# Performance work log

Measured on AMD Instinct MI355X. Metric: run time of the kernel, lower is better.

The kernel has to match this reference:

```python
import jax, jax.numpy as jnp
import numpy as np

N_NODES = 30000
IN_DIM = 8
HIDDEN = 64
HEADS1 = 8
OUT_DIM = 8
NEG_SLOPE = 0.2


def _glorot(key, shape):
    fan_in, fan_out = shape[0], shape[-1]
    lim = jnp.sqrt(6.0 / (fan_in + fan_out))
    return jax.random.uniform(key, shape, jnp.float32, -lim, lim)


def setup_inputs() -> dict:
    key = jax.random.key(0)
    ks = jax.random.split(key, 12)
    x = jax.random.normal(ks[0], (N_NODES, IN_DIM), jnp.float32)
    edge_index = jax.random.randint(ks[1], (2, 300000), 0, N_NODES, jnp.int32)
    # layer 1: in=8, out=HIDDEN per head, 8 heads, concat
    W1l = _glorot(ks[2], (IN_DIM, HEADS1 * HIDDEN))
    W1r = _glorot(ks[3], (IN_DIM, HEADS1 * HIDDEN))
    a1 = _glorot(ks[4], (HEADS1, HIDDEN))
    b1 = jnp.zeros((HEADS1 * HIDDEN,), jnp.float32)
    # layer 2: in=HEADS1*HIDDEN, out=OUT_DIM, 1 head
    W2l = _glorot(ks[5], (HEADS1 * HIDDEN, OUT_DIM))
    W2r = _glorot(ks[6], (HEADS1 * HIDDEN, OUT_DIM))
    a2 = _glorot(ks[7], (1, OUT_DIM))
    b2 = jnp.zeros((OUT_DIM,), jnp.float32)
    return {"x": x, "edge_index": edge_index, "W1l": W1l, "W1r": W1r,
            "a1": a1, "b1": b1, "W2l": W2l, "W2r": W2r, "a2": a2, "b2": b2}


def gatv2_layer(x, src, dst, Wl, Wr, att, bias, heads, out_ch):
    n = x.shape[0]
    xl = (x @ Wl).reshape(n, heads, out_ch)   # messages (source side)
    xr = (x @ Wr).reshape(n, heads, out_ch)   # target side
    h = jax.nn.leaky_relu(xl[src] + xr[dst], NEG_SLOPE)   # [E,H,C]
    e = jnp.einsum('ehc,hc->eh', h, att)                  # [E,H]
    # segment softmax over incoming edges per destination node
    m = jax.ops.segment_max(e, dst, num_segments=n)
    p = jnp.exp(e - m[dst])
    denom = jax.ops.segment_sum(p, dst, num_segments=n)
    alpha = p / denom[dst]                                # [E,H]
    out = jax.ops.segment_sum(alpha[..., None] * xl[src], dst, num_segments=n)
    return out.reshape(n, heads * out_ch) + bias


def reference(x, edge_index, W1l, W1r, a1, b1, W2l, W2r, a2, b2):
    n = x.shape[0]
    loops = jnp.arange(n, dtype=edge_index.dtype)
    src = jnp.concatenate([edge_index[0], loops])  # add_self_loops=True (PyG default)
    dst = jnp.concatenate([edge_index[1], loops])
    h = gatv2_layer(x, src, dst, W1l, W1r, a1, b1, HEADS1, HIDDEN)
    h = jax.nn.relu(h)
    out = gatv2_layer(h, src, dst, W2l, W2r, a2, b2, 1, OUT_DIM)
    return out
```

## Files before the change

kernel.cpp:

```cpp
#include <hip/hip_runtime.h>
#include <hip/hip_fp16.h>
#include <math.h>

#define N_NODES   30000
#define N_EDGE    300000
#define N_EDGE_T  330000
#define HEADS     8
#define HIDDEN    64
#define IN_DIM    8
#define OUT_DIM   8
#define NEG_SLOPE 0.2f

#define DPP_ADDF(x, ctrl)                                                     \
    x += __int_as_float(__builtin_amdgcn_update_dpp(                          \
            0, __float_as_int(x), (ctrl), 0xF, 0xF, true))
#define RED16(x) do { DPP_ADDF(x, 0xB1); DPP_ADDF(x, 0x4E);                   \
                      DPP_ADDF(x, 0x141); DPP_ADDF(x, 0x140); } while (0)
#define RED8(x)  do { DPP_ADDF(x, 0xB1); DPP_ADDF(x, 0x4E);                   \
                      DPP_ADDF(x, 0x141); } while (0)


__global__ __launch_bounds__(256) void zero_kernel(int* __restrict__ count) {
    int i = blockIdx.x * 256 + threadIdx.x;
    if (i < N_NODES) count[i] = 0;
}

__global__ __launch_bounds__(256) void count_kernel(const int* __restrict__ ei,
                                                    int* __restrict__ count) {
    int e = blockIdx.x * 256 + threadIdx.x;
    if (e >= N_EDGE_T) return;
    int d = (e < N_EDGE) ? ei[N_EDGE + e] : (e - N_EDGE);
    atomicAdd(&count[d], 1);
}

__global__ __launch_bounds__(1024) void scan_kernel(const int* __restrict__ count,
                                                    int* __restrict__ row_start,
                                                    int* __restrict__ cursor) {
    __shared__ int wsum[16];
    const int tid  = threadIdx.x;
    const int wave = tid >> 6;
    const int lane = tid & 63;
    const int4* c4 = (const int4*)count;
    const int N4 = N_NODES / 4;
    int run = 0;
    for (int r = 0; r < 4; ++r) {
        const int g  = r * 1024 + tid;
        const int i0 = 2 * g;
        const int i1 = 2 * g + 1;
        int4 v0 = make_int4(0,0,0,0), v1 = make_int4(0,0,0,0);
        if (i0 < N4) v0 = c4[i0];
        if (i1 < N4) v1 = c4[i1];
        int s = v0.x + v0.y + v0.z + v0.w + v1.x + v1.y + v1.z + v1.w;
        int sc = s;
        #pragma unroll
        for (int off = 1; off < 64; off <<= 1) {
            int t = __shfl_up(sc, off, 64);
            if (lane >= off) sc += t;
        }
        if (lane == 63) wsum[wave] = sc;
        __syncthreads();
        if (tid < 16) {
            int w = wsum[tid];
            #pragma unroll
            for (int off = 1; off < 16; off <<= 1) {
                int t = __shfl_up(w, off, 64);
                if (tid >= off) w += t;
            }
            wsum[tid] = w;
        }
        __syncthreads();
        const int woff = (wave > 0) ? wsum[wave - 1] : 0;
        int e0 = run + woff + (sc - s);
        int4 ex0, ex1;
        ex0.x = e0;           ex0.y = ex0.x + v0.x;
        ex0.z = ex0.y + v0.y; ex0.w = ex0.z + v0.z;
        int e4 = ex0.w + v0.w;
        ex1.x = e4;           ex1.y = ex1.x + v1.x;
        ex1.z = ex1.y + v1.y; ex1.w = ex1.z + v1.z;
        if (i0 < N4) { ((int4*)row_start)[i0] = ex0; ((int4*)cursor)[i0] = ex0; }
        if (i1 < N4) { ((int4*)row_start)[i1] = ex1; ((int4*)cursor)[i1] = ex1; }
        const int tot = wsum[15];
        __syncthreads();
        run += tot;
    }
    if (tid == 0) row_start[N_NODES] = run;
}

__global__ __launch_bounds__(256) void scatter_kernel(const int* __restrict__ ei,
                                                      int* __restrict__ cursor,
                                                      int* __restrict__ edge_src) {
    int e = blockIdx.x * 256 + threadIdx.x;
    if (e >= N_EDGE_T) return;
    int s, d;
    if (e < N_EDGE) { s = ei[e]; d = ei[N_EDGE + e]; }
    else            { s = d = e - N_EDGE; }
    int pos = atomicAdd(&cursor[d], 1);
    edge_src[pos] = s;
}


__global__ __launch_bounds__(256) void proj_kernel(
    const float* __restrict__ x, const float* __restrict__ W1l,
    __half* __restrict__ xl_h)
{
    const int t = threadIdx.x;
    float w0[IN_DIM], w1[IN_DIM];
    #pragma unroll
    for (int k = 0; k < IN_DIM; ++k) {
        const float2 wp = *(const float2*)&W1l[k * 512 + 2 * t];
        w0[k] = wp.x; w1[k] = wp.y;
    }
    for (int n = blockIdx.x; n < N_NODES; n += gridDim.x) {
        float xv[IN_DIM];
        #pragma unroll
        for (int k = 0; k < IN_DIM; ++k) xv[k] = x[n * IN_DIM + k];
        float l0 = 0.f, l1 = 0.f;
        #pragma unroll
        for (int k = 0; k < IN_DIM; ++k) {
            l0 = fmaf(xv[k], w0[k], l0);
            l1 = fmaf(xv[k], w1[k], l1);
        }
        ((__half2*)xl_h)[n * 256 + t] = __floats2half2_rn(l0, l1);
    }
}


__global__ void __launch_bounds__(256, 4)
layer1_kernel(
    const float* __restrict__ x,
    const __half* __restrict__ xl_h, const float* __restrict__ W1r,
    const float* __restrict__ a1,  const float* __restrict__ b1,
    const float* __restrict__ W2l, const float* __restrict__ W2r,
    const int* __restrict__ row_start, const int* __restrict__ edge_src,
    float* __restrict__ xl2, float* __restrict__ xr2)
{
    const int wv   = threadIdx.x >> 6;
    const int lane = threadIdx.x & 63;
    const int d    = blockIdx.x * 4 + wv;
    const int colb = lane * 8;

    float av[8], xr[8];
    { const float4 a0 = *(const float4*)&a1[colb];
      const float4 a4 = *(const float4*)&a1[colb + 4];
      av[0]=a0.x; av[1]=a0.y; av[2]=a0.z; av[3]=a0.w;
      av[4]=a4.x; av[5]=a4.y; av[6]=a4.z; av[7]=a4.w; }
    #pragma unroll
    for (int i = 0; i < 8; ++i) xr[i] = 0.f;
    #pragma unroll
    for (int k = 0; k < IN_DIM; ++k) {
        const float4 r0 = *(const float4*)&W1r[k * 512 + colb];
        const float4 r4 = *(const float4*)&W1r[k * 512 + colb + 4];
        const float xv = x[d * IN_DIM + k];
        xr[0] = fmaf(xv, r0.x, xr[0]); xr[1] = fmaf(xv, r0.y, xr[1]);
        xr[2] = fmaf(xv, r0.z, xr[2]); xr[3] = fmaf(xv, r0.w, xr[3]);
        xr[4] = fmaf(xv, r4.x, xr[4]); xr[5] = fmaf(xv, r4.y, xr[5]);
        xr[6] = fmaf(xv, r4.z, xr[6]); xr[7] = fmaf(xv, r4.w, xr[7]);
    }

    const int rs = row_start[d];
    const int re = row_start[d + 1];

    float denom  = 0.f;
    float acc[8] = {0.f,0.f,0.f,0.f,0.f,0.f,0.f,0.f};

    auto ldrow = [&](int s, float (&o)[8]) {
        const int4 r = *(const int4*)(xl_h + (size_t)s * 512 + colb);
        union { int i; __half2 h; } u0, u1, u2, u3;
        u0.i = r.x; u1.i = r.y; u2.i = r.z; u3.i = r.w;
        float2 f;
        f = __half22float2(u0.h); o[0] = f.x; o[1] = f.y;
        f = __half22float2(u1.h); o[2] = f.x; o[3] = f.y;
        f = __half22float2(u2.h); o[4] = f.x; o[5] = f.y;
        f = __half22float2(u3.h); o[6] = f.x; o[7] = f.y;
    };

    auto edge1 = [&](const float (&rr)[8], bool valid) {
        float e = 0.f;
        #pragma unroll
        for (int i = 0; i < 8; ++i) {
            const float q = rr[i] + xr[i];
            const float t = fmaxf(q, NEG_SLOPE * q);
            e = fmaf(av[i], t, e);
        }
        RED8(e);
        const float p = valid ? __expf(e) : 0.f;
        denom += p;
        #pragma unroll
        for (int i = 0; i < 8; ++i) acc[i] = fmaf(p, rr[i], acc[i]);
    };

    float RA[8], RB[8];
    {
        const int sA = edge_src[rs];
        const bool vB0 = rs + 1 < re;
        const int sB = edge_src[vB0 ? rs + 1 : rs];
        ldrow(sA, RA); ldrow(sB, RB);
    }
    bool vB = rs + 1 < re;

    for (int base = rs;;) {
        const int  nb   = base + 2;
        const bool more = nb < re;
        float RC[8], RD[8];
        bool vD = false;
        if (more) {
            const int sC = edge_src[nb];
            vD = nb + 1 < re;
            const int sD = edge_src[vD ? nb + 1 : nb];
            ldrow(sC, RC); ldrow(sD, RD);
        }
        edge1(RA, true);
        edge1(RB, vB);
        if (!more) break;
        #pragma unroll
        for (int i = 0; i < 8; ++i) { RA[i] = RC[i]; RB[i] = RD[i]; }
        vB = vD;
        base = nb;
    }

    const float inv = 1.f / denom;
    float hv[8];
    { const float4 b0 = *(const float4*)&b1[colb];
      const float4 b4 = *(const float4*)&b1[colb + 4];
      hv[0] = fmaxf(fmaf(acc[0], inv, b0.x), 0.f);
      hv[1] = fmaxf(fmaf(acc[1], inv, b0.y), 0.f);
      hv[2] = fmaxf(fmaf(acc[2], inv, b0.z), 0.f);
      hv[3] = fmaxf(fmaf(acc[3], inv, b0.w), 0.f);
      hv[4] = fmaxf(fmaf(acc[4], inv, b4.x), 0.f);
      hv[5] = fmaxf(fmaf(acc[5], inv, b4.y), 0.f);
      hv[6] = fmaxf(fmaf(acc[6], inv, b4.z), 0.f);
      hv[7] = fmaxf(fmaf(acc[7], inv, b4.w), 0.f); }

    float vl[OUT_DIM], vr[OUT_DIM];
    #pragma unroll
    for (int j = 0; j < OUT_DIM; ++j) { vl[j] = 0.f; vr[j] = 0.f; }
    #pragma unroll
    for (int i = 0; i < 8; ++i) {
        const int c = colb + i;
        const float4 l0 = *(const float4*)&W2l[c * OUT_DIM];
        const float4 l1 = *(const float4*)&W2l[c * OUT_DIM + 4];
        const float4 r0 = *(const float4*)&W2r[c * OUT_DIM];
        const float4 r1 = *(const float4*)&W2r[c * OUT_DIM + 4];
        const float h = hv[i];
        vl[0] = fmaf(h, l0.x, vl[0]); vl[1] = fmaf(h, l0.y, vl[1]);
        vl[2] = fmaf(h, l0.z, vl[2]); vl[3] = fmaf(h, l0.w, vl[3]);
        vl[4] = fmaf(h, l1.x, vl[4]); vl[5] = fmaf(h, l1.y, vl[5]);
        vl[6] = fmaf(h, l1.z, vl[6]); vl[7] = fmaf(h, l1.w, vl[7]);
        vr[0] = fmaf(h, r0.x, vr[0]); vr[1] = fmaf(h, r0.y, vr[1]);
        vr[2] = fmaf(h, r0.z, vr[2]); vr[3] = fmaf(h, r0.w, vr[3]);
        vr[4] = fmaf(h, r1.x, vr[4]); vr[5] = fmaf(h, r1.y, vr[5]);
        vr[6] = fmaf(h, r1.z, vr[6]); vr[7] = fmaf(h, r1.w, vr[7]);
    }
    #pragma unroll
    for (int j = 0; j < OUT_DIM; ++j) {
        RED16(vl[j]);
        vl[j] += __shfl_xor(vl[j], 16, 64);
        vl[j] += __shfl_xor(vl[j], 32, 64);
        RED16(vr[j]);
        vr[j] += __shfl_xor(vr[j], 16, 64);
        vr[j] += __shfl_xor(vr[j], 32, 64);
    }
    if (lane == 0) {
        *(float4*)&xl2[d * OUT_DIM]     = make_float4(vl[0], vl[1], vl[2], vl[3]);
        *(float4*)&xl2[d * OUT_DIM + 4] = make_float4(vl[4], vl[5], vl[6], vl[7]);
        *(float4*)&xr2[d * OUT_DIM]     = make_float4(vr[0], vr[1], vr[2], vr[3]);
        *(float4*)&xr2[d * OUT_DIM + 4] = make_float4(vr[4], vr[5], vr[6], vr[7]);
    }
}


__global__ __launch_bounds__(256) void layer2_kernel(
    const float* __restrict__ xl2, const float* __restrict__ xr2,
    const float* __restrict__ a2,  const float* __restrict__ b2,
    const int* __restrict__ row_start, const int* __restrict__ edge_src,
    float* __restrict__ out)
{
    const int wave = threadIdx.x >> 6;
    const int lane = threadIdx.x & 63;
    const int d = blockIdx.x * 4 + wave;
    if (d >= N_NODES) return;
    const int sub = lane >> 3;
    const int c   = lane & 7;

    const float a_c  = a2[c];
    const float xr_d = xr2[d * OUT_DIM + c];

    const int rs = row_start[d];
    const int re = row_start[d + 1];

    int  e0 = rs + sub;      const bool v0 = e0 < re; e0 = v0 ? e0 : re - 1;
    int  e1 = rs + 8 + sub;  const bool v1 = e1 < re; e1 = v1 ? e1 : re - 1;
    const int s0 = edge_src[e0];
    const int s1 = edge_src[e1];
    const float x0 = xl2[s0 * OUT_DIM + c];
    const float x1 = xl2[s1 * OUT_DIM + c];

    const float u0 = x0 + xr_d; const float t0 = fmaxf(u0, NEG_SLOPE * u0);
    const float u1 = x1 + xr_d; const float t1 = fmaxf(u1, NEG_SLOPE * u1);
    float g0 = a_c * t0;
    float g1 = a_c * t1;
    RED8(g0); RED8(g1);
    const float p0 = v0 ? __expf(g0) : 0.f;
    const float p1 = v1 ? __expf(g1) : 0.f;
    float denom = p0 + p1;
    float acc   = fmaf(p1, x1, p0 * x0);

    for (int b = rs + 16; b < re; b += 8) {
        int e = b + sub;
        const bool v = e < re; e = v ? e : re - 1;
        const int s = edge_src[e];
        const float xs = xl2[s * OUT_DIM + c];
        const float u = xs + xr_d;
        const float t = fmaxf(u, NEG_SLOPE * u);
        float g = a_c * t;
        RED8(g);
        const float p = v ? __expf(g) : 0.f;
        denom += p;
        acc = fmaf(p, xs, acc);
    }

    denom += __shfl_xor(denom, 8,  64);  acc += __shfl_xor(acc, 8,  64);
    denom += __shfl_xor(denom, 16, 64);  acc += __shfl_xor(acc, 16, 64);
    denom += __shfl_xor(denom, 32, 64);  acc += __shfl_xor(acc, 32, 64);

    if (sub == 0) out[d * OUT_DIM + c] = acc / denom + b2[c];
}


extern "C" void kernel_launch(void* const* d_in, const int* in_sizes, int n_in,
                              void* d_out, int out_size, void* d_ws, size_t ws_size,
                              hipStream_t stream) {
    const float* x   = (const float*)d_in[0];
    const int*   ei  = (const int*)  d_in[1];
    const float* W1l = (const float*)d_in[2];
    const float* W1r = (const float*)d_in[3];
    const float* a1  = (const float*)d_in[4];
    const float* b1  = (const float*)d_in[5];
    const float* W2l = (const float*)d_in[6];
    const float* W2r = (const float*)d_in[7];
    const float* a2  = (const float*)d_in[8];
    const float* b2  = (const float*)d_in[9];
    float* out = (float*)d_out;

    char* ws = (char*)d_ws;
    size_t off = 0;
    auto carve = [&](size_t bytes) { char* p = ws + off; off += (bytes + 255) & ~size_t(255); return p; };
    int*    count     = (int*)   carve(N_NODES * sizeof(int));
    int*    row_start = (int*)   carve((N_NODES + 1) * sizeof(int));
    int*    cursor    = (int*)   carve(N_NODES * sizeof(int));
    int*    edge_src  = (int*)   carve(N_EDGE_T * sizeof(int));
    float*  xl2       = (float*) carve(N_NODES * OUT_DIM * sizeof(float));
    float*  xr2       = (float*) carve(N_NODES * OUT_DIM * sizeof(float));
    __half* xl_h      = (__half*)carve((size_t)N_NODES * 512 * sizeof(__half));

    proj_kernel   <<<1024, 256, 0, stream>>>(x, W1l, xl_h);
    zero_kernel   <<<(N_NODES  + 255) / 256, 256, 0, stream>>>(count);
    count_kernel  <<<(N_EDGE_T + 255) / 256, 256, 0, stream>>>(ei, count);
    scan_kernel   <<<1, 1024, 0, stream>>>(count, row_start, cursor);
    scatter_kernel<<<(N_EDGE_T + 255) / 256, 256, 0, stream>>>(ei, cursor, edge_src);
    layer1_kernel <<<N_NODES / 4, 256, 0, stream>>>(x, xl_h, W1r, a1, b1, W2l, W2r,
                                                    row_start, edge_src, xl2, xr2);
    layer2_kernel <<<(N_NODES + 3) / 4, 256, 0, stream>>>(xl2, xr2, a2, b2,
                                                          row_start, edge_src, out);
}
```

Baseline: 299.5 us.

## Preload edge indices per lane and deepen layer1 gather prefetch to four rows

Layer1 now loads up to 64 edge source indices cooperatively, one per lane, and broadcasts them with shuffles, so the dependent edge_src loads are gone from the gather loop. The software pipeline is widened from two to four prefetched half-precision rows, kept as raw int4 until use, with a scheduling barrier between the loads and the compute. Node features x and row_start bounds are also loaded once per lane and shuffled instead of each lane loading every value. This adds register pressure and a scalar fallback loop for nodes with more than 64 incoming edges.

```diff
diff --git a/kernel.cpp b/kernel.cpp
--- a/kernel.cpp
+++ b/kernel.cpp
@@ -103,7 +103,8 @@
     const float* __restrict__ x, const float* __restrict__ W1l,
     __half* __restrict__ xl_h)
 {
-    const int t = threadIdx.x;
+    const int t    = threadIdx.x;
+    const int lane = t & 63;
     float w0[IN_DIM], w1[IN_DIM];
     #pragma unroll
     for (int k = 0; k < IN_DIM; ++k) {
@@ -111,14 +112,13 @@
         w0[k] = wp.x; w1[k] = wp.y;
     }
     for (int n = blockIdx.x; n < N_NODES; n += gridDim.x) {
-        float xv[IN_DIM];
-        #pragma unroll
-        for (int k = 0; k < IN_DIM; ++k) xv[k] = x[n * IN_DIM + k];
+        const float xlane = x[n * IN_DIM + (lane & 7)];
         float l0 = 0.f, l1 = 0.f;
         #pragma unroll
         for (int k = 0; k < IN_DIM; ++k) {
-            l0 = fmaf(xv[k], w0[k], l0);
-            l1 = fmaf(xv[k], w1[k], l1);
+            const float xk = __shfl(xlane, k, 64);
+            l0 = fmaf(xk, w0[k], l0);
+            l1 = fmaf(xk, w1[k], l1);
         }
         ((__half2*)xl_h)[n * 256 + t] = __floats2half2_rn(l0, l1);
     }
@@ -139,6 +139,16 @@
     const int d    = blockIdx.x * 4 + wv;
     const int colb = lane * 8;
 
+    const int rse = row_start[d + (lane & 1)];
+    const int rs  = __shfl(rse, 0, 64);
+    const int re  = __shfl(rse, 1, 64);
+    const int deg = re - rs;
+    const int nb  = deg < 64 ? deg : 64;
+
+    const int eidx = edge_src[rs + (lane < deg ? lane : deg - 1)];
+
+    const float xlane = x[d * IN_DIM + (lane & 7)];
+
     float av[8], xr[8];
     { const float4 a0 = *(const float4*)&a1[colb];
       const float4 a4 = *(const float4*)&a1[colb + 4];
@@ -148,33 +158,30 @@
     for (int i = 0; i < 8; ++i) xr[i] = 0.f;
     #pragma unroll
     for (int k = 0; k < IN_DIM; ++k) {
+        const float xv = __shfl(xlane, k, 64);
         const float4 r0 = *(const float4*)&W1r[k * 512 + colb];
         const float4 r4 = *(const float4*)&W1r[k * 512 + colb + 4];
-        const float xv = x[d * IN_DIM + k];
         xr[0] = fmaf(xv, r0.x, xr[0]); xr[1] = fmaf(xv, r0.y, xr[1]);
         xr[2] = fmaf(xv, r0.z, xr[2]); xr[3] = fmaf(xv, r0.w, xr[3]);
         xr[4] = fmaf(xv, r4.x, xr[4]); xr[5] = fmaf(xv, r4.y, xr[5]);
         xr[6] = fmaf(xv, r4.z, xr[6]); xr[7] = fmaf(xv, r4.w, xr[7]);
     }
 
-    const int rs = row_start[d];
-    const int re = row_start[d + 1];
-
     float denom  = 0.f;
     float acc[8] = {0.f,0.f,0.f,0.f,0.f,0.f,0.f,0.f};
 
-    auto ldrow = [&](int s, float (&o)[8]) {
-        const int4 r = *(const int4*)(xl_h + (size_t)s * 512 + colb);
+    auto ldraw = [&](int j) -> int4 {
+        const int s = __shfl(eidx, j, 64);
+        return *(const int4*)(xl_h + (size_t)s * 512 + colb);
+    };
+    auto edge1 = [&](const int4 r, bool valid) {
         union { int i; __half2 h; } u0, u1, u2, u3;
         u0.i = r.x; u1.i = r.y; u2.i = r.z; u3.i = r.w;
-        float2 f;
-        f = __half22float2(u0.h); o[0] = f.x; o[1] = f.y;
-        f = __half22float2(u1.h); o[2] = f.x; o[3] = f.y;
-        f = __half22float2(u2.h); o[4] = f.x; o[5] = f.y;
-        f = __half22float2(u3.h); o[6] = f.x; o[7] = f.y;
-    };
-
-    auto edge1 = [&](const float (&rr)[8], bool valid) {
+        float rr[8]; float2 f;
+        f = __half22float2(u0.h); rr[0] = f.x; rr[1] = f.y;
+        f = __half22float2(u1.h); rr[2] = f.x; rr[3] = f.y;
+        f = __half22float2(u2.h); rr[4] = f.x; rr[5] = f.y;
+        f = __half22float2(u3.h); rr[6] = f.x; rr[7] = f.y;
         float e = 0.f;
         #pragma unroll
         for (int i = 0; i < 8; ++i) {
@@ -189,33 +196,37 @@
         for (int i = 0; i < 8; ++i) acc[i] = fmaf(p, rr[i], acc[i]);
     };
 
-    float RA[8], RB[8];
+    int4 R0, R1, R2, R3;
     {
-        const int sA = edge_src[rs];
-        const bool vB0 = rs + 1 < re;
-        const int sB = edge_src[vB0 ? rs + 1 : rs];
-        ldrow(sA, RA); ldrow(sB, RB);
-    }
-    bool vB = rs + 1 < re;
-
-    for (int base = rs;;) {
-        const int  nb   = base + 2;
-        const bool more = nb < re;
-        float RC[8], RD[8];
-        bool vD = false;
+        const int m = nb - 1;
+        R0 = ldraw(0);
+        R1 = ldraw(1 < m ? 1 : m);
+        R2 = ldraw(2 < m ? 2 : m);
+        R3 = ldraw(3 < m ? 3 : m);
+    }
+    for (int j = 0;; j += 4) {
+        const bool more = j + 4 < nb;
+        int4 N0, N1, N2, N3;
         if (more) {
-            const int sC = edge_src[nb];
-            vD = nb + 1 < re;
-            const int sD = edge_src[vD ? nb + 1 : nb];
-            ldrow(sC, RC); ldrow(sD, RD);
-        }
-        edge1(RA, true);
-        edge1(RB, vB);
+            const int m = nb - 1;
+            const int j4 = j + 4;
+            N0 = ldraw(j4 < m ? j4 : m);
+            N1 = ldraw(j4 + 1 < m ? j4 + 1 : m);
+            N2 = ldraw(j4 + 2 < m ? j4 + 2 : m);
+            N3 = ldraw(j4 + 3 < m ? j4 + 3 : m);
+            __builtin_amdgcn_sched_barrier(0);
+        }
+        edge1(R0, true);
+        edge1(R1, j + 1 < nb);
+        edge1(R2, j + 2 < nb);
+        edge1(R3, j + 3 < nb);
         if (!more) break;
-        #pragma unroll
-        for (int i = 0; i < 8; ++i) { RA[i] = RC[i]; RB[i] = RD[i]; }
-        vB = vD;
-        base = nb;
+        R0 = N0; R1 = N1; R2 = N2; R3 = N3;
+    }
+    for (int j = 64; j < deg; ++j) {
+        const int s = edge_src[rs + j];
+        const int4 r = *(const int4*)(xl_h + (size_t)s * 512 + colb);
+        edge1(r, true);
     }
 
     const float inv = 1.f / denom;
@@ -282,11 +293,12 @@
     const int sub = lane >> 3;
     const int c   = lane & 7;
 
+    const int rse = row_start[d + (lane & 1)];
+    const int rs  = __shfl(rse, 0, 64);
+    const int re  = __shfl(rse, 1, 64);
+
     const float a_c  = a2[c];
     const float xr_d = xr2[d * OUT_DIM + c];
-
-    const int rs = row_start[d];
-    const int re = row_start[d + 1];
 
     int  e0 = rs + sub;      const bool v0 = e0 < re; e0 = v0 ? e0 : re - 1;
     int  e1 = rs + 8 + sub;  const bool v1 = e1 < re; e1 = v1 ? e1 : re - 1;
```

New measurement: 292.6 us. -2.3%, faster.
